# Performance work log

Measured on AMD Instinct MI355X. Metric: run time of the kernel, lower is better.

Reference implementation:

```python
import jax, jax.numpy as jnp
import numpy as np

IGNORE_INDEX = -100


def setup_inputs() -> dict:
    key = jax.random.key(0)
    k1, k2, k3 = jax.random.split(key, 3)
    B, S, D, V = 4, 2048, 2048, 32000
    hidden_states = jax.random.normal(k1, (B, S, D), dtype=jnp.float32)
    lm_head_weight = jax.random.normal(k2, (V, D), dtype=jnp.float32) * (D ** -0.5)
    labels = jax.random.randint(k3, (B, S), 0, V, dtype=jnp.int64)
    return {"hidden_states": hidden_states, "lm_head_weight": lm_head_weight, "labels": labels}


def reference(hidden_states, lm_head_weight, labels):
    D = hidden_states.shape[-1]
    # causal LM shift: predict token t+1 from hidden state t
    h = hidden_states[..., :-1, :].astype(jnp.float32).reshape(-1, D)   # [N, D]
    t = labels[..., 1:].reshape(-1)                                     # [N]
    w = lm_head_weight.astype(jnp.float32)                              # [V, D]

    logits = jnp.einsum("nd,vd->nv", h, w)                              # [N, V]
    lse = jax.nn.logsumexp(logits, axis=-1)                             # [N]

    valid = t != IGNORE_INDEX
    safe_t = jnp.where(valid, t, 0)
    gold = jnp.take_along_axis(logits, safe_t[:, None], axis=-1)[:, 0]  # [N]

    nll = jnp.where(valid, lse - gold, 0.0)
    n_valid = jnp.maximum(jnp.sum(valid.astype(jnp.float32)), 1.0)
    return jnp.sum(nll) / n_valid
```

## Files before the change

### kernel.cpp

```cpp
#include <hip/hip_runtime.h>
#include <stdint.h>

#define IGNORE_INDEX (-100)

typedef __attribute__((ext_vector_type(8))) short bf16x8;
typedef __attribute__((ext_vector_type(4))) float f32x4;

static constexpr int Bv = 4, Sv = 2048, Dv = 2048, Vv = 32000;
static constexpr int Nv = Bv * (Sv - 1);
static constexpr int NP = 8192;
static constexpr int BM = 256;
static constexpr int BK = 64;
static constexpr int NT = Dv / BK;

typedef const __attribute__((address_space(1))) unsigned int* gptr_t;
typedef __attribute__((address_space(3))) unsigned int* lptr_t;

__device__ __forceinline__ unsigned short f2bf(float f) {
    unsigned int u = __float_as_uint(f);
    u += 0x7fffu + ((u >> 16) & 1u);
    return (unsigned short)(u >> 16);
}

__global__ void convert_w_kernel(const float* __restrict__ w,
                                 unsigned short* __restrict__ wbf) {
    int i = blockIdx.x * blockDim.x + threadIdx.x;
    const float4 v = ((const float4*)w)[i];
    ushort4 o;
    o.x = f2bf(v.x); o.y = f2bf(v.y); o.z = f2bf(v.z); o.w = f2bf(v.w);
    ((ushort4*)wbf)[i] = o;
}

__global__ void convert_h_kernel(const float* __restrict__ h,
                                 unsigned short* __restrict__ hbf) {
    int i = blockIdx.x * blockDim.x + threadIdx.x;
    int e0 = i * 4;
    int n = e0 >> 11;
    int d = e0 & 2047;
    ushort4 o;
    if (n < Nv) {
        int b = n / 2047;
        int s = n - b * 2047;
        const float4 v = *(const float4*)(h + ((size_t)b * Sv + s) * Dv + d);
        o.x = f2bf(v.x); o.y = f2bf(v.y); o.z = f2bf(v.z); o.w = f2bf(v.w);
    } else {
        o.x = 0; o.y = 0; o.z = 0; o.w = 0;
    }
    ((ushort4*)hbf)[i] = o;
}

__global__ void prep_meta_kernel(const int* __restrict__ labels,
                                 int* __restrict__ t,
                                 float* __restrict__ sumexp,
                                 float* __restrict__ gold) {
    int n = blockIdx.x * blockDim.x + threadIdx.x;
    if (n >= NP) return;
    sumexp[n] = 0.0f;
    gold[n] = 0.0f;
    int tv = IGNORE_INDEX;
    if (n < Nv) {
        int b = n / 2047;
        int s = n - b * 2047;
        tv = labels[b * Sv + s + 1];
    }
    t[n] = tv;
}

__global__ __launch_bounds__(512, 2)
void ce_gemm(const unsigned short* __restrict__ hbf,
             const unsigned short* __restrict__ wbf,
             const int* __restrict__ t,
             float* __restrict__ sumexp,
             float* __restrict__ gold) {
    __shared__ unsigned short lds_a[2][BM * BK];
    __shared__ unsigned short lds_b[2][BM * BK];
    __shared__ float lds_rowsum[BM];
    __shared__ int lds_t[BM];

    const int tid  = threadIdx.x;
    const int lane = tid & 63;
    const int wave = tid >> 6;
    const int wr   = wave >> 2;
    const int wc   = wave & 3;
    const int quad = lane >> 4;
    const int l15  = lane & 15;
    const int R0   = blockIdx.x * BM;
    const int C0   = blockIdx.y * BM;

    f32x4 acc[8][4];
    const f32x4 z = {0.f, 0.f, 0.f, 0.f};
#pragma unroll
    for (int mi = 0; mi < 8; ++mi)
#pragma unroll
        for (int ni = 0; ni < 4; ++ni)
            acc[mi][ni] = z;

    const int ld_r = tid >> 3;
    const int jg   = (tid & 7) ^ (ld_r & 7);
    const unsigned short* ga = hbf + (size_t)(R0 + ld_r) * Dv + jg * 8;
    const unsigned short* gb = wbf + (size_t)(C0 + ld_r) * Dv + jg * 8;

#define STAGE_HALF(DSTARR, GBASE, KT, H)                                    \
    do {                                                                    \
        _Pragma("unroll")                                                   \
        for (int _i = 2 * (H); _i < 2 * (H) + 2; ++_i) {                    \
            __builtin_amdgcn_global_load_lds(                               \
                (gptr_t)((GBASE) + (size_t)_i * 64 * Dv + (KT) * BK),       \
                (lptr_t)(&DSTARR[tid * 8 + _i * 4096]), 16, 0, 0);          \
        }                                                                   \
    } while (0)

#define LDSF(BASE, R, C) \
    (*(const bf16x8*)((BASE) + (R) * BK + (((C) ^ ((R) & 7)) * 8)))

#define VM6 asm volatile("s_waitcnt vmcnt(6)" ::: "memory")
#define VM0 asm volatile("s_waitcnt vmcnt(0)" ::: "memory")
#define NOVM ((void)0)

#define PHASE(ABUF, Q, LOADB, BBUF, VMW, ...)                               \
    do {                                                                    \
        bf16x8 a0_, a1_, a2_, a3_;                                          \
        {                                                                   \
            const int r0_ = (2 * (Q)) * 32 + wr * 16 + l15;                 \
            const int r1_ = (2 * (Q) + 1) * 32 + wr * 16 + l15;             \
            const unsigned short* ab_ = &lds_a[ABUF][0];                    \
            a0_ = LDSF(ab_, r0_, quad);                                     \
            a1_ = LDSF(ab_, r0_, quad + 4);                                 \
            a2_ = LDSF(ab_, r1_, quad);                                     \
            a3_ = LDSF(ab_, r1_, quad + 4);                                 \
        }                                                                   \
        if (LOADB) {                                                        \
            const unsigned short* bb_ = &lds_b[BBUF][0];                    \
            _Pragma("unroll")                                               \
            for (int ni_ = 0; ni_ < 4; ++ni_) {                             \
                const int br_ = wc * 64 + ni_ * 16 + l15;                   \
                bfr[ni_][0] = LDSF(bb_, br_, quad);                         \
                bfr[ni_][1] = LDSF(bb_, br_, quad + 4);                     \
            }                                                               \
        }                                                                   \
        __VA_ARGS__;                                                        \
        __builtin_amdgcn_s_barrier();                                       \
        asm volatile("s_waitcnt lgkmcnt(0)" ::: "memory");                  \
        __builtin_amdgcn_sched_barrier(0);                                  \
        __builtin_amdgcn_s_setprio(1);                                      \
        {                                                                   \
            const int miA_ = 2 * (Q), miB_ = 2 * (Q) + 1;                   \
            _Pragma("unroll")                                               \
            for (int ni_ = 0; ni_ < 4; ++ni_) {                             \
                acc[miA_][ni_] = __builtin_amdgcn_mfma_f32_16x16x32_bf16(   \
                    a0_, bfr[ni_][0], acc[miA_][ni_], 0, 0, 0);             \
                acc[miA_][ni_] = __builtin_amdgcn_mfma_f32_16x16x32_bf16(   \
                    a1_, bfr[ni_][1], acc[miA_][ni_], 0, 0, 0);             \
            }                                                               \
            _Pragma("unroll")                                               \
            for (int ni_ = 0; ni_ < 4; ++ni_) {                             \
                acc[miB_][ni_] = __builtin_amdgcn_mfma_f32_16x16x32_bf16(   \
                    a2_, bfr[ni_][0], acc[miB_][ni_], 0, 0, 0);             \
                acc[miB_][ni_] = __builtin_amdgcn_mfma_f32_16x16x32_bf16(   \
                    a3_, bfr[ni_][1], acc[miB_][ni_], 0, 0, 0);             \
            }                                                               \
        }                                                                   \
        __builtin_amdgcn_s_setprio(0);                                      \
        VMW;                                                                \
        __builtin_amdgcn_s_barrier();                                       \
    } while (0)

    bf16x8 bfr[4][2];

    STAGE_HALF(lds_a[0], ga, 0, 0);
    STAGE_HALF(lds_a[0], ga, 0, 1);
    STAGE_HALF(lds_b[0], gb, 0, 0);
    STAGE_HALF(lds_b[0], gb, 0, 1);
    STAGE_HALF(lds_b[1], gb, 1, 0);
    STAGE_HALF(lds_b[1], gb, 1, 1);
    STAGE_HALF(lds_a[1], ga, 1, 0);
    VM6;
    __builtin_amdgcn_s_barrier();

#pragma unroll 1
    for (int j = 0; j < 15; ++j) {
        const int t1 = 2 * j + 1, t2 = 2 * j + 2, t3 = 2 * j + 3;
        PHASE(0, 0, 1, 0, NOVM, STAGE_HALF(lds_a[1], ga, t1, 1));
        PHASE(0, 1, 0, 0, NOVM, STAGE_HALF(lds_b[0], gb, t2, 0));
        PHASE(0, 2, 0, 0, NOVM, STAGE_HALF(lds_b[0], gb, t2, 1));
        PHASE(0, 3, 0, 0, VM6,  STAGE_HALF(lds_a[0], ga, t2, 0));
        PHASE(1, 0, 1, 1, NOVM, STAGE_HALF(lds_a[0], ga, t2, 1));
        PHASE(1, 1, 0, 1, NOVM, STAGE_HALF(lds_b[1], gb, t3, 0));
        PHASE(1, 2, 0, 1, NOVM, STAGE_HALF(lds_b[1], gb, t3, 1));
        PHASE(1, 3, 0, 1, VM6,  STAGE_HALF(lds_a[1], ga, t3, 0));
    }
    PHASE(0, 0, 1, 0, NOVM, STAGE_HALF(lds_a[1], ga, 31, 1));
    PHASE(0, 1, 0, 0, NOVM, NOVM);
    PHASE(0, 2, 0, 0, NOVM, NOVM);
    PHASE(0, 3, 0, 0, VM0,  NOVM);
    PHASE(1, 0, 1, 1, NOVM, NOVM);
    PHASE(1, 1, 0, 1, NOVM, NOVM);
    PHASE(1, 2, 0, 1, NOVM, NOVM);
    PHASE(1, 3, 0, 1, NOVM, NOVM);

#undef PHASE
#undef STAGE_HALF

    if (tid < BM) {
        lds_rowsum[tid] = 0.0f;
        lds_t[tid] = t[R0 + tid];
    }
    __syncthreads();

#pragma unroll
    for (int mi = 0; mi < 8; ++mi) {
#pragma unroll
        for (int reg = 0; reg < 4; ++reg) {
            const int lrow = mi * 32 + wr * 16 + quad * 4 + reg;
            const int grow = R0 + lrow;
            const int lbl  = lds_t[lrow];
            float s = 0.0f;
#pragma unroll
            for (int ni = 0; ni < 4; ++ni) {
                const float v = acc[mi][ni][reg];
                s += __expf(v);
                const int gcol = C0 + wc * 64 + ni * 16 + l15;
                if (lbl == gcol) gold[grow] = v;
            }
#pragma unroll
            for (int off = 1; off < 16; off <<= 1)
                s += __shfl_xor(s, off, 64);
            if (l15 == 0) atomicAdd(&lds_rowsum[lrow], s);
        }
    }
    __syncthreads();
    if (tid < BM) {
        const int grow = R0 + tid;
        if (grow < Nv) atomicAdd(&sumexp[grow], lds_rowsum[tid]);
    }
}

__global__ void ce_finalize(const float* __restrict__ sumexp,
                            const float* __restrict__ gold,
                            const int* __restrict__ t,
                            float* __restrict__ out) {
    __shared__ float ssum[4];
    __shared__ float scnt[4];
    float s = 0.0f, cnt = 0.0f;
    for (int n = threadIdx.x; n < Nv; n += 256) {
        if (t[n] != IGNORE_INDEX) {
            s += logf(sumexp[n]) - gold[n];
            cnt += 1.0f;
        }
    }
#pragma unroll
    for (int off = 32; off > 0; off >>= 1) {
        s += __shfl_down(s, off, 64);
        cnt += __shfl_down(cnt, off, 64);
    }
    const int wid = threadIdx.x >> 6;
    if ((threadIdx.x & 63) == 0) { ssum[wid] = s; scnt[wid] = cnt; }
    __syncthreads();
    if (threadIdx.x == 0) {
        float S = 0.0f, C = 0.0f;
        for (int i = 0; i < 4; ++i) { S += ssum[i]; C += scnt[i]; }
        out[0] = S / fmaxf(C, 1.0f);
    }
}

extern "C" void kernel_launch(void* const* d_in, const int* in_sizes, int n_in,
                              void* d_out, int out_size, void* d_ws, size_t ws_size,
                              hipStream_t stream) {
    const float* h      = (const float*)d_in[0];
    const float* w      = (const float*)d_in[1];
    const int*   labels = (const int*)d_in[2];
    float* out = (float*)d_out;

    char* ws = (char*)d_ws;
    unsigned short* hbf = (unsigned short*)ws;
    unsigned short* wbf = (unsigned short*)(ws + (size_t)NP * Dv * 2);
    char* tail = ws + (size_t)NP * Dv * 2 + (size_t)Vv * Dv * 2;
    float* sumexp = (float*)tail;
    float* gold   = (float*)(tail + (size_t)NP * 4);
    int*   t      = (int*)(tail + (size_t)NP * 8);

    hipLaunchKernelGGL(convert_w_kernel, dim3((Vv * Dv / 4) / 256), dim3(256), 0, stream, w, wbf);
    hipLaunchKernelGGL(convert_h_kernel, dim3((NP * Dv / 4) / 256), dim3(256), 0, stream, h, hbf);
    hipLaunchKernelGGL(prep_meta_kernel, dim3(NP / 256), dim3(256), 0, stream, labels, t, sumexp, gold);
    hipLaunchKernelGGL(ce_gemm, dim3(NP / BM, Vv / BM), dim3(512), 0, stream,
                       hbf, wbf, t, sumexp, gold);
    hipLaunchKernelGGL(ce_finalize, dim3(1), dim3(256), 0, stream, sumexp, gold, t, out);
}
```

Measured before the change: 1.392 ms.

## Double-buffer LDS fragment registers across phases and swizzle workgroup order

Restructures the GEMM main loop so each phase issues LDS reads for the next phase's A/B fragments into alternate register sets while running MFMAs on the current ones. Partial lgkmcnt waits let those reads overlap compute, and the global-load wait points are rebalanced. It also remaps the flat workgroup id with an 8-way interleave, changing which tiles run concurrently to improve cache locality. This costs more VGPRs, which could cause spills at launch bounds (512,2), and the waitcnt bookkeeping is fragile.

```diff
diff --git a/kernel.cpp b/kernel.cpp
--- a/kernel.cpp
+++ b/kernel.cpp
@@ -84,8 +84,13 @@
     const int wc   = wave & 3;
     const int quad = lane >> 4;
     const int l15  = lane & 15;
-    const int R0   = blockIdx.x * BM;
-    const int C0   = blockIdx.y * BM;
+
+    const int GX  = NP / BM;
+    const int nwg = GX * (Vv / BM);
+    int fid = blockIdx.y * GX + blockIdx.x;
+    fid = (fid & 7) * (nwg >> 3) + (fid >> 3);
+    const int R0 = (fid & (GX - 1)) * BM;
+    const int C0 = (fid / GX) * BM;
 
     f32x4 acc[8][4];
     const f32x4 z = {0.f, 0.f, 0.f, 0.f};
@@ -113,94 +118,110 @@
 #define LDSF(BASE, R, C) \
     (*(const bf16x8*)((BASE) + (R) * BK + (((C) ^ ((R) & 7)) * 8)))
 
+#define VM8 asm volatile("s_waitcnt vmcnt(8)" ::: "memory")
 #define VM6 asm volatile("s_waitcnt vmcnt(6)" ::: "memory")
+#define VM4 asm volatile("s_waitcnt vmcnt(4)" ::: "memory")
 #define VM0 asm volatile("s_waitcnt vmcnt(0)" ::: "memory")
 #define NOVM ((void)0)
-
-#define PHASE(ABUF, Q, LOADB, BBUF, VMW, ...)                               \
+#define NOSTG ((void)0)
+
+#define PHASE(QM, AU, QR, ARB, AL, BU, LB, BRB, BL, LGKM, VMW, STG)         \
     do {                                                                    \
-        bf16x8 a0_, a1_, a2_, a3_;                                          \
-        {                                                                   \
-            const int r0_ = (2 * (Q)) * 32 + wr * 16 + l15;                 \
-            const int r1_ = (2 * (Q) + 1) * 32 + wr * 16 + l15;             \
-            const unsigned short* ab_ = &lds_a[ABUF][0];                    \
-            a0_ = LDSF(ab_, r0_, quad);                                     \
-            a1_ = LDSF(ab_, r0_, quad + 4);                                 \
-            a2_ = LDSF(ab_, r1_, quad);                                     \
-            a3_ = LDSF(ab_, r1_, quad + 4);                                 \
-        }                                                                   \
-        if (LOADB) {                                                        \
-            const unsigned short* bb_ = &lds_b[BBUF][0];                    \
+        STG;                                                                \
+        if ((QR) >= 0) {                                                    \
+            const unsigned short* ab_ = &lds_a[ARB][0];                     \
+            const int r0_ = (QR) * 64 + wr * 16 + l15;                      \
+            AL[0] = LDSF(ab_, r0_, quad);                                   \
+            AL[1] = LDSF(ab_, r0_, quad + 4);                               \
+            AL[2] = LDSF(ab_, r0_ + 32, quad);                              \
+            AL[3] = LDSF(ab_, r0_ + 32, quad + 4);                          \
+        }                                                                   \
+        if (LB) {                                                           \
+            const unsigned short* bb_ = &lds_b[BRB][0];                     \
             _Pragma("unroll")                                               \
             for (int ni_ = 0; ni_ < 4; ++ni_) {                             \
                 const int br_ = wc * 64 + ni_ * 16 + l15;                   \
-                bfr[ni_][0] = LDSF(bb_, br_, quad);                         \
-                bfr[ni_][1] = LDSF(bb_, br_, quad + 4);                     \
+                BL[ni_][0] = LDSF(bb_, br_, quad);                          \
+                BL[ni_][1] = LDSF(bb_, br_, quad + 4);                      \
             }                                                               \
         }                                                                   \
-        __VA_ARGS__;                                                        \
         __builtin_amdgcn_s_barrier();                                       \
-        asm volatile("s_waitcnt lgkmcnt(0)" ::: "memory");                  \
+        asm volatile("s_waitcnt lgkmcnt(" LGKM ")" ::: "memory");           \
         __builtin_amdgcn_sched_barrier(0);                                  \
         __builtin_amdgcn_s_setprio(1);                                      \
-        {                                                                   \
-            const int miA_ = 2 * (Q), miB_ = 2 * (Q) + 1;                   \
-            _Pragma("unroll")                                               \
-            for (int ni_ = 0; ni_ < 4; ++ni_) {                             \
-                acc[miA_][ni_] = __builtin_amdgcn_mfma_f32_16x16x32_bf16(   \
-                    a0_, bfr[ni_][0], acc[miA_][ni_], 0, 0, 0);             \
-                acc[miA_][ni_] = __builtin_amdgcn_mfma_f32_16x16x32_bf16(   \
-                    a1_, bfr[ni_][1], acc[miA_][ni_], 0, 0, 0);             \
-            }                                                               \
-            _Pragma("unroll")                                               \
-            for (int ni_ = 0; ni_ < 4; ++ni_) {                             \
-                acc[miB_][ni_] = __builtin_amdgcn_mfma_f32_16x16x32_bf16(   \
-                    a2_, bfr[ni_][0], acc[miB_][ni_], 0, 0, 0);             \
-                acc[miB_][ni_] = __builtin_amdgcn_mfma_f32_16x16x32_bf16(   \
-                    a3_, bfr[ni_][1], acc[miB_][ni_], 0, 0, 0);             \
-            }                                                               \
+        _Pragma("unroll")                                                   \
+        for (int ni_ = 0; ni_ < 4; ++ni_) {                                 \
+            acc[2*(QM)][ni_] = __builtin_amdgcn_mfma_f32_16x16x32_bf16(     \
+                AU[0], BU[ni_][0], acc[2*(QM)][ni_], 0, 0, 0);              \
+            acc[2*(QM)][ni_] = __builtin_amdgcn_mfma_f32_16x16x32_bf16(     \
+                AU[1], BU[ni_][1], acc[2*(QM)][ni_], 0, 0, 0);              \
+        }                                                                   \
+        _Pragma("unroll")                                                   \
+        for (int ni_ = 0; ni_ < 4; ++ni_) {                                 \
+            acc[2*(QM)+1][ni_] = __builtin_amdgcn_mfma_f32_16x16x32_bf16(   \
+                AU[2], BU[ni_][0], acc[2*(QM)+1][ni_], 0, 0, 0);            \
+            acc[2*(QM)+1][ni_] = __builtin_amdgcn_mfma_f32_16x16x32_bf16(   \
+                AU[3], BU[ni_][1], acc[2*(QM)+1][ni_], 0, 0, 0);            \
         }                                                                   \
         __builtin_amdgcn_s_setprio(0);                                      \
         VMW;                                                                \
         __builtin_amdgcn_s_barrier();                                       \
     } while (0)
 
-    bf16x8 bfr[4][2];
-
+    bf16x8 aE[4], aO[4];
+    bf16x8 bE[4][2], bO[4][2];
+
+    STAGE_HALF(lds_b[0], gb, 0, 0);
+    STAGE_HALF(lds_b[0], gb, 0, 1);
     STAGE_HALF(lds_a[0], ga, 0, 0);
     STAGE_HALF(lds_a[0], ga, 0, 1);
-    STAGE_HALF(lds_b[0], gb, 0, 0);
-    STAGE_HALF(lds_b[0], gb, 0, 1);
     STAGE_HALF(lds_b[1], gb, 1, 0);
     STAGE_HALF(lds_b[1], gb, 1, 1);
     STAGE_HALF(lds_a[1], ga, 1, 0);
-    VM6;
+    asm volatile("s_waitcnt vmcnt(6)" ::: "memory");
     __builtin_amdgcn_s_barrier();
+
+    {
+        const unsigned short* ab_ = &lds_a[0][0];
+        const int r0_ = 0 * 64 + wr * 16 + l15;
+        aE[0] = LDSF(ab_, r0_, quad);
+        aE[1] = LDSF(ab_, r0_, quad + 4);
+        aE[2] = LDSF(ab_, r0_ + 32, quad);
+        aE[3] = LDSF(ab_, r0_ + 32, quad + 4);
+        const unsigned short* bb_ = &lds_b[0][0];
+#pragma unroll
+        for (int ni_ = 0; ni_ < 4; ++ni_) {
+            const int br_ = wc * 64 + ni_ * 16 + l15;
+            bE[ni_][0] = LDSF(bb_, br_, quad);
+            bE[ni_][1] = LDSF(bb_, br_, quad + 4);
+        }
+    }
 
 #pragma unroll 1
     for (int j = 0; j < 15; ++j) {
         const int t1 = 2 * j + 1, t2 = 2 * j + 2, t3 = 2 * j + 3;
-        PHASE(0, 0, 1, 0, NOVM, STAGE_HALF(lds_a[1], ga, t1, 1));
-        PHASE(0, 1, 0, 0, NOVM, STAGE_HALF(lds_b[0], gb, t2, 0));
-        PHASE(0, 2, 0, 0, NOVM, STAGE_HALF(lds_b[0], gb, t2, 1));
-        PHASE(0, 3, 0, 0, VM6,  STAGE_HALF(lds_a[0], ga, t2, 0));
-        PHASE(1, 0, 1, 1, NOVM, STAGE_HALF(lds_a[0], ga, t2, 1));
-        PHASE(1, 1, 0, 1, NOVM, STAGE_HALF(lds_b[1], gb, t3, 0));
-        PHASE(1, 2, 0, 1, NOVM, STAGE_HALF(lds_b[1], gb, t3, 1));
-        PHASE(1, 3, 0, 1, VM6,  STAGE_HALF(lds_a[1], ga, t3, 0));
-    }
-    PHASE(0, 0, 1, 0, NOVM, STAGE_HALF(lds_a[1], ga, 31, 1));
-    PHASE(0, 1, 0, 0, NOVM, NOVM);
-    PHASE(0, 2, 0, 0, NOVM, NOVM);
-    PHASE(0, 3, 0, 0, VM0,  NOVM);
-    PHASE(1, 0, 1, 1, NOVM, NOVM);
-    PHASE(1, 1, 0, 1, NOVM, NOVM);
-    PHASE(1, 2, 0, 1, NOVM, NOVM);
-    PHASE(1, 3, 0, 1, NOVM, NOVM);
+        PHASE(0, aE, 1, 0, aO, bE, 0, 0, bO, "4",  VM8,  STAGE_HALF(lds_a[1], ga, t1, 1));
+        PHASE(1, aO, 2, 0, aE, bE, 0, 0, bO, "4",  NOVM, STAGE_HALF(lds_b[0], gb, t2, 0));
+        PHASE(2, aE, 3, 0, aO, bE, 0, 0, bO, "4",  VM4,  STAGE_HALF(lds_b[0], gb, t2, 1));
+        PHASE(3, aO, 0, 1, aE, bE, 1, 1, bO, "12", NOVM, STAGE_HALF(lds_a[0], ga, t2, 0));
+        PHASE(0, aE, 1, 1, aO, bO, 0, 0, bE, "4",  NOVM, STAGE_HALF(lds_a[0], ga, t2, 1));
+        PHASE(1, aO, 2, 1, aE, bO, 0, 0, bE, "4",  NOVM, STAGE_HALF(lds_b[1], gb, t3, 0));
+        PHASE(2, aE, 3, 1, aO, bO, 0, 0, bE, "4",  VM6,  STAGE_HALF(lds_b[1], gb, t3, 1));
+        PHASE(3, aO, 0, 0, aE, bO, 1, 0, bE, "12", NOVM, STAGE_HALF(lds_a[1], ga, t3, 0));
+    }
+    PHASE(0, aE, 1, 0, aO, bE, 0, 0, bO, "4",  VM8,  STAGE_HALF(lds_a[1], ga, 31, 1));
+    PHASE(1, aO, 2, 0, aE, bE, 0, 0, bO, "4",  NOVM, NOSTG);
+    PHASE(2, aE, 3, 0, aO, bE, 0, 0, bO, "4",  VM0,  NOSTG);
+    PHASE(3, aO, 0, 1, aE, bE, 1, 1, bO, "12", NOVM, NOSTG);
+    PHASE(0, aE, 1, 1, aO, bO, 0, 0, bE, "4",  NOVM, NOSTG);
+    PHASE(1, aO, 2, 1, aE, bO, 0, 0, bE, "4",  NOVM, NOSTG);
+    PHASE(2, aE, 3, 1, aO, bO, 0, 0, bE, "4",  NOVM, NOSTG);
+    PHASE(3, aO, -1, 0, aE, bO, 0, 0, bE, "0", NOVM, NOSTG);
 
 #undef PHASE
 #undef STAGE_HALF
 
+    __syncthreads();
     if (tid < BM) {
         lds_rowsum[tid] = 0.0f;
         lds_t[tid] = t[R0 + tid];
```

Result: slower. 1.506 ms (+8.1%).
